# Performance work log

Measured on AMD Instinct MI355X. Metric: run time of the kernel, lower is better.

## Reference

```python
import jax, jax.numpy as jnp
import numpy as np

B, L, C, D, H = 32, 4096, 64, 512, 720
EPS = 1e-5

def _xavier(key, shape):
    fan_in, fan_out = shape
    lim = float(np.sqrt(6.0 / (fan_in + fan_out)))
    return jax.random.uniform(key, shape, minval=-lim, maxval=lim, dtype=jnp.float32)

def setup_inputs() -> dict:
    key = jax.random.key(0)
    ks = jax.random.split(key, 8)
    return {
        "x": jax.random.normal(ks[0], (B, L, C), dtype=jnp.float32),
        "alpha": jnp.full((C,), 0.5, dtype=jnp.float32),
        "rev_w": jnp.ones((C,), dtype=jnp.float32),
        "rev_b": jnp.zeros((C,), dtype=jnp.float32),
        "se_w": _xavier(ks[1], (C, D)), "se_b": jnp.zeros((D,), jnp.float32),
        "sp_w": _xavier(ks[2], (D, C)), "sp_b": jnp.zeros((C,), jnp.float32),
        "st_w": _xavier(ks[3], (L, H)), "st_b": jnp.zeros((H,), jnp.float32),
        "te_w": _xavier(ks[4], (C, D)), "te_b": jnp.zeros((D,), jnp.float32),
        "tp_w": _xavier(ks[5], (D, C)), "tp_b": jnp.zeros((C,), jnp.float32),
        "tt_w": _xavier(ks[6], (L, H)), "tt_b": jnp.zeros((H,), jnp.float32),
    }

def _path(z, ew, eb, pw, pb, tw, tb):
    # z: (B,L,C) -> embed C->D -> (identity backbone) -> proj D->C -> temporal L->H
    h = z @ ew + eb            # (B,L,D)
    h = h @ pw + pb            # (B,L,C)
    h = jnp.einsum('blc,lh->bhc', h, tw) + tb[None, :, None]  # (B,H,C)
    return h

def reference(x, alpha, rev_w, rev_b, se_w, se_b, sp_w, sp_b, st_w, st_b,
              te_w, te_b, tp_w, tp_b, tt_w, tt_b):
    # RevIN norm (stats detached, var unbiased=False)
    mean = jax.lax.stop_gradient(jnp.mean(x, axis=1, keepdims=True))          # (B,1,C)
    stdev = jax.lax.stop_gradient(jnp.sqrt(jnp.var(x, axis=1, keepdims=True) + EPS))
    xn = (x - mean) / stdev * rev_w + rev_b
    # EMA decomposition: trend[t] = a*trend[t-1] + (1-a)*x[t], trend[0]=x[0]
    a = jax.nn.sigmoid(alpha)  # (C,)
    def step(carry, xt):
        nxt = a * carry + (1.0 - a) * xt
        return nxt, nxt
    t0 = xn[:, 0]                                    # (B,C)
    _, tr = jax.lax.scan(step, t0, jnp.swapaxes(xn, 0, 1)[1:])  # (L-1,B,C)
    trend = jnp.swapaxes(jnp.concatenate([t0[None], tr], axis=0), 0, 1)  # (B,L,C)
    seasonal = xn - trend
    out = _path(seasonal, se_w, se_b, sp_w, sp_b, st_w, st_b) \
        + _path(trend,    te_w, te_b, tp_w, tp_b, tt_w, tt_b)   # (B,H,C)
    # RevIN denorm
    out = (out - rev_b) / (rev_w + EPS)
    out = out * stdev + mean
    return out
```

## Files before the change

### kernel.cpp

```cpp
#include <hip/hip_runtime.h>
#include <hip/hip_bf16.h>
#include <string.h>
#include <stdint.h>

typedef __hip_bfloat16 bf16_t;
typedef float f32x4 __attribute__((ext_vector_type(4)));
typedef short bf16x8 __attribute__((ext_vector_type(8)));

static constexpr int Bn = 32, Ln = 4096, Cn = 64, Hn = 720, HPn = 768;
static constexpr float EPSf = 1e-5f;

static constexpr size_t OSR_SLICE = (size_t)Bn * Hn * Cn;

__device__ __forceinline__ short f2bf(float f) {
  bf16_t h = __float2bfloat16(f);
  unsigned short u; memcpy(&u, &h, 2);
  return (short)u;
}

__device__ __forceinline__ float sigm(float v) { return 1.f / (1.f + expf(-v)); }

__global__ void __launch_bounds__(256) k_preA(
    const float* __restrict__ st_w, const float* __restrict__ tt_w,
    const float* __restrict__ x, const float* __restrict__ alpha,
    bf16_t* __restrict__ Wt, float* __restrict__ Spart,
    float* __restrict__ Psub, float* __restrict__ Pseg,
    float* __restrict__ Ssum, float* __restrict__ Ssq) {
  __shared__ __align__(16) char smem[20736];
  int bid = blockIdx.x, t = threadIdx.x;

  if (bid < 1536) {
    float (*tile)[65] = (float(*)[65])smem;
    float (*cs16)[64] = (float(*)[64])(smem + 16640);
    int p = bid / 768, rem = bid % 768;
    int lc = rem & 63, hc = rem >> 6;
    const float* W = p ? tt_w : st_w;
    int l0 = lc * 64, h0 = hc * 64;
    int g16 = t >> 4, c4l = (t & 15) * 4;
    int h = h0 + c4l;
    f32x4 ps = (f32x4){0.f, 0.f, 0.f, 0.f};
#pragma unroll
    for (int rr = 0; rr < 4; ++rr) {
      int r = rr * 16 + g16;
      const float* src = &W[(size_t)(l0 + r) * Hn + h];
      f32x4 v;
      if (h + 3 < Hn) {
        v = *reinterpret_cast<const f32x4*>(src);
      } else {
#pragma unroll
        for (int i = 0; i < 4; ++i) v[i] = (h + i < Hn) ? src[i] : 0.f;
      }
      tile[r][c4l + 0] = v[0]; tile[r][c4l + 1] = v[1];
      tile[r][c4l + 2] = v[2]; tile[r][c4l + 3] = v[3];
      ps += v;
    }
    *reinterpret_cast<f32x4*>(&cs16[g16][c4l]) = ps;
    __syncthreads();
    if (t < 64) {
      float s = 0.f;
#pragma unroll
      for (int g = 0; g < 16; ++g) s += cs16[g][t];
      Spart[((size_t)p * 64 + lc) * 768 + h0 + t] = s;
    }
    short* AF = (short*)Wt + (size_t)p * HPn * Ln;
#pragma unroll
    for (int u = 0; u < 2; ++u) {
      int uid = u * 256 + t;
      int ln = uid & 63, ktl = (uid >> 6) & 1, htl = uid >> 7;
      int fr = ln & 15, hi = ln >> 4;
      int ll = ktl * 32 + hi * 8;
      int hh = htl * 16 + fr;
      bf16x8 v;
#pragma unroll
      for (int e = 0; e < 8; ++e) v[e] = f2bf(tile[ll + e][hh]);
      size_t ht = (size_t)(h0 >> 4) + htl, ktg = (size_t)(l0 >> 5) + ktl;
      *reinterpret_cast<bf16x8*>(&AF[((ht * 128 + ktg) << 9) + ((size_t)ln << 3)]) = v;
    }
  } else {
    float (*lp)[64] = (float(*)[64])smem;
    float (*ls)[64] = (float(*)[64])(smem + 4096);
    float (*lq)[64] = (float(*)[64])(smem + 8192);
    int idx = bid - 1536;
    int b = idx >> 4, sg = idx & 15;
    int ty = t >> 6, tx = t & 63;
    int s = sg * 4 + ty;
    int c4 = (tx & 15) * 4, sub = tx >> 4;
    float a[4], k1[4];
#pragma unroll
    for (int i = 0; i < 4; ++i) { a[i] = sigm(alpha[c4 + i]); k1[i] = 1.f - a[i]; }
    const float* xb = x + ((size_t)b * Ln + s * 64 + sub * 16) * Cn + c4;
    float pr[4] = {0.f, 0.f, 0.f, 0.f}, sm[4] = {0.f, 0.f, 0.f, 0.f}, sq[4] = {0.f, 0.f, 0.f, 0.f};
#pragma unroll
    for (int j = 0; j < 16; ++j) {
      f32x4 v = *reinterpret_cast<const f32x4*>(xb + (size_t)j * Cn);
#pragma unroll
      for (int i = 0; i < 4; ++i) {
        sm[i] += v[i];
        sq[i] = fmaf(v[i], v[i], sq[i]);
        pr[i] = fmaf(a[i], pr[i], k1[i] * v[i]);
      }
    }
    *reinterpret_cast<f32x4*>(&Psub[(((size_t)b * 64 + s) * 4 + sub) * 64 + c4]) =
        (f32x4){pr[0], pr[1], pr[2], pr[3]};
#pragma unroll
    for (int i = 0; i < 4; ++i) {
      lp[ty * 4 + sub][c4 + i] = pr[i];
      ls[ty * 4 + sub][c4 + i] = sm[i];
      lq[ty * 4 + sub][c4 + i] = sq[i];
    }
    __syncthreads();
    int c = tx;
    float av = sigm(alpha[c]);
    float a16 = av * av; a16 *= a16; a16 *= a16; a16 *= a16;
    float P = ((lp[ty * 4 + 0][c] * a16 + lp[ty * 4 + 1][c]) * a16 + lp[ty * 4 + 2][c]) * a16 + lp[ty * 4 + 3][c];
    int oidx = (b * 64 + s) * 64 + c;
    Pseg[oidx] = P;
    Ssum[oidx] = ls[ty * 4 + 0][c] + ls[ty * 4 + 1][c] + ls[ty * 4 + 2][c] + ls[ty * 4 + 3][c];
    Ssq[oidx]  = lq[ty * 4 + 0][c] + lq[ty * 4 + 1][c] + lq[ty * 4 + 2][c] + lq[ty * 4 + 3][c];
  }
}

__global__ void __launch_bounds__(256) k_mid(
    const float* __restrict__ x, const float* __restrict__ alpha,
    const float* __restrict__ rev_w, const float* __restrict__ rev_b,
    const float* __restrict__ Pseg, const float* __restrict__ Ssum, const float* __restrict__ Ssq,
    const float* __restrict__ se_w, const float* __restrict__ sp_w,
    const float* __restrict__ se_b, const float* __restrict__ sp_b,
    const float* __restrict__ te_w, const float* __restrict__ tp_w,
    const float* __restrict__ te_b, const float* __restrict__ tp_b,
    const float* __restrict__ Spart,
    float* __restrict__ mean, float* __restrict__ rstd, float* __restrict__ stdv,
    float* __restrict__ CarryIn, float* __restrict__ M, float* __restrict__ cvec,
    float* __restrict__ S) {
  __shared__ __align__(16) char smem[35072];
  int bid = blockIdx.x, t = threadIdx.x;

  if (bid < 8) {
    int b = bid * 4 + (t >> 6), c = t & 63;
    float sm = 0.f, sq = 0.f;
#pragma unroll 8
    for (int s = 0; s < 64; ++s) {
      int idx = (b * 64 + s) * 64 + c;
      sm += Ssum[idx]; sq += Ssq[idx];
    }
    float mn = sm * (1.f / 4096.f);
    float var = sq * (1.f / 4096.f) - mn * mn;
    float sd = sqrtf(var + EPSf);
    float rs = 1.f / sd;
    mean[b * 64 + c] = mn; stdv[b * 64 + c] = sd; rstd[b * 64 + c] = rs;

    float w = rev_w[c], rb = rev_b[c];
    float g = rs * w, d = rb - mn * g;
    float a = sigm(alpha[c]);
    float a2 = a * a, a4 = a2 * a2, a8 = a4 * a4, a16 = a8 * a8, a32 = a16 * a16;
    float a64 = a32 * a32;
    float dk1s = d * (1.f - a64);
    float carry = fmaf(g, x[((size_t)b * Ln) * Cn + c], d);
    for (int so = 0; so < 8; ++so) {
      float pv[8];
#pragma unroll
      for (int i = 0; i < 8; ++i)
        pv[i] = Pseg[((size_t)(b * 64 + so * 8 + i)) * 64 + c];
#pragma unroll
      for (int i = 0; i < 8; ++i) {
        CarryIn[((size_t)(b * 64 + so * 8 + i)) * 64 + c] = carry;
        carry = fmaf(a64, carry, fmaf(g, pv[i], dk1s));
      }
    }
  } else if (bid < 10) {
    float (*ews)[68] = (float(*)[68])smem;
    float (*pws)[68] = (float(*)[68])(smem + 17408);
    float* ebs = (float*)(smem + 34816);
    int p = bid - 8;
    const float* ew = p ? te_w : se_w;
    const float* pw = p ? tp_w : sp_w;
    const float* eb = p ? te_b : se_b;
    const float* pb = p ? tp_b : sp_b;
    int r0 = (t >> 4) * 4, c0 = (t & 15) * 4;
    float acc[4][4];
#pragma unroll
    for (int i = 0; i < 4; ++i)
#pragma unroll
      for (int j = 0; j < 4; ++j) acc[i][j] = 0.f;
    float cv = 0.f;
    for (int dc = 0; dc < 8; ++dc) {
      int d0 = dc * 64;
#pragma unroll
      for (int q = 0; q < 4; ++q) {
        int fi = t * 4 + q;
        int r = fi >> 4, dd = (fi * 4) & 63;
        *reinterpret_cast<f32x4*>(&ews[r][dd]) = *reinterpret_cast<const f32x4*>(&ew[r * 512 + d0 + dd]);
        *reinterpret_cast<f32x4*>(&pws[r][dd]) = *reinterpret_cast<const f32x4*>(&pw[(d0 + r) * 64 + dd]);
      }
      if (t < 64) ebs[t] = eb[d0 + t];
      __syncthreads();
#pragma unroll 4
      for (int g = 0; g < 16; ++g) {
        int dd = g * 4;
        f32x4 av[4], bv[4];
#pragma unroll
        for (int i = 0; i < 4; ++i) av[i] = *reinterpret_cast<const f32x4*>(&ews[r0 + i][dd]);
#pragma unroll
        for (int d = 0; d < 4; ++d) bv[d] = *reinterpret_cast<const f32x4*>(&pws[dd + d][c0]);
#pragma unroll
        for (int d = 0; d < 4; ++d)
#pragma unroll
          for (int i = 0; i < 4; ++i)
#pragma unroll
            for (int j = 0; j < 4; ++j) acc[i][j] = fmaf(av[i][d], bv[d][j], acc[i][j]);
      }
      if (t < 64) {
#pragma unroll 8
        for (int dd = 0; dd < 64; ++dd) cv = fmaf(ebs[dd], pws[dd][t], cv);
      }
      __syncthreads();
    }
#pragma unroll
    for (int i = 0; i < 4; ++i)
#pragma unroll
      for (int j = 0; j < 4; ++j)
        M[p * 4096 + (r0 + i) * 64 + c0 + j] = acc[i][j];
    if (t < 64) cvec[p * 64 + t] = cv + pb[t];
  } else {
    int idx = (bid - 10) * 256 + t;
    int p = idx / 768, h = idx % 768;
    float s = 0.f;
#pragma unroll 8
    for (int lc = 0; lc < 64; ++lc)
      s += Spart[((size_t)p * 64 + lc) * 768 + h];
    S[p * 768 + h] = s;
  }
}

__global__ void __launch_bounds__(256) k_scanC(const float* __restrict__ x, const float* __restrict__ alpha,
                                               const float* __restrict__ rev_w, const float* __restrict__ rev_b,
                                               const float* __restrict__ mean, const float* __restrict__ rstd,
                                               const float* __restrict__ CarryIn, const float* __restrict__ Psub,
                                               bf16_t* __restrict__ Zt) {
  int b = blockIdx.x, ty = threadIdx.y, s = blockIdx.y * 4 + ty, t = threadIdx.x;
  int c4 = (t & 15) * 4, sub = t >> 4;
  float g[4], d[4], a[4], k1[4], a16[4], dk[4], tr[4];
#pragma unroll
  for (int i = 0; i < 4; ++i) {
    int c = c4 + i;
    float rs = rstd[b * 64 + c];
    g[i] = rs * rev_w[c]; d[i] = rev_b[c] - mean[b * 64 + c] * g[i];
    a[i] = sigm(alpha[c]); k1[i] = 1.f - a[i];
    float v = a[i] * a[i]; v *= v; v *= v; v *= v;
    a16[i] = v;
    dk[i] = d[i] * (1.f - v);
  }
  f32x4 cs = *reinterpret_cast<const f32x4*>(&CarryIn[((size_t)b * 64 + s) * 64 + c4]);
#pragma unroll
  for (int i = 0; i < 4; ++i) tr[i] = cs[i];
  for (int k = 0; k < sub; ++k) {
    f32x4 p = *reinterpret_cast<const f32x4*>(&Psub[(((size_t)b * 64 + s) * 4 + k) * 64 + c4]);
#pragma unroll
    for (int i = 0; i < 4; ++i) tr[i] = fmaf(a16[i], tr[i], fmaf(g[i], p[i], dk[i]));
  }
  const float* xb = x + ((size_t)b * Ln + s * 64 + sub * 16) * Cn + c4;
  bf16x8 vs[4][2], vt[4][2];
#pragma unroll
  for (int j = 0; j < 16; ++j) {
    f32x4 v = *reinterpret_cast<const f32x4*>(xb + (size_t)j * Cn);
#pragma unroll
    for (int i = 0; i < 4; ++i) {
      float xn = fmaf(g[i], v[i], d[i]);
      tr[i] = fmaf(a[i], tr[i], k1[i] * xn);
      vs[i][j >> 3][j & 7] = f2bf(xn - tr[i]);
      vt[i][j >> 3][j & 7] = f2bf(tr[i]);
    }
  }
  __shared__ short stage[4][8][520];
  short* BF0 = (short*)Zt;
  const size_t PATH = (size_t)Bn * Cn * Ln;
  int cq = (t & 15) >> 2;
  int u = cq * 2 + (sub >> 1);
  int hb = (sub & 1) * 2;
#pragma unroll
  for (int i = 0; i < 4; ++i) {
    int frv = (c4 & 15) + i;
    *reinterpret_cast<bf16x8*>(&stage[ty][u][(hb * 16 + frv) * 8]) = vs[i][0];
    *reinterpret_cast<bf16x8*>(&stage[ty][u][((hb + 1) * 16 + frv) * 8]) = vs[i][1];
  }
#pragma unroll
  for (int uu = 0; uu < 8; ++uu) {
    size_t nt = (size_t)b * 4 + (uu >> 1), ktg = (size_t)s * 2 + (uu & 1);
    *reinterpret_cast<bf16x8*>(BF0 + ((nt * 128 + ktg) << 9) + ((size_t)t << 3)) =
        *reinterpret_cast<const bf16x8*>(&stage[ty][uu][t * 8]);
  }
#pragma unroll
  for (int i = 0; i < 4; ++i) {
    int frv = (c4 & 15) + i;
    *reinterpret_cast<bf16x8*>(&stage[ty][u][(hb * 16 + frv) * 8]) = vt[i][0];
    *reinterpret_cast<bf16x8*>(&stage[ty][u][((hb + 1) * 16 + frv) * 8]) = vt[i][1];
  }
#pragma unroll
  for (int uu = 0; uu < 8; ++uu) {
    size_t nt = (size_t)b * 4 + (uu >> 1), ktg = (size_t)s * 2 + (uu & 1);
    *reinterpret_cast<bf16x8*>(BF0 + PATH + ((nt * 128 + ktg) << 9) + ((size_t)t << 3)) =
        *reinterpret_cast<const bf16x8*>(&stage[ty][uu][t * 8]);
  }
}

template <int KS>
__global__ void __launch_bounds__(256, 3) k_gemm(const bf16_t* __restrict__ Wt, const bf16_t* __restrict__ Zt,
                                                 float* __restrict__ Osr) {
  int per = gridDim.x >> 3;
  int swz = (blockIdx.x & 7) * per + (blockIdx.x >> 3);
  int z = swz / 96, rem = swz % 96;
  int by = rem >> 4, bx = rem & 15;
  int p = z / KS, kq = z % KS;
  const short* AF = (const short*)Wt + (size_t)p * HPn * Ln;
  const short* BF = (const short*)Zt + (size_t)p * (Bn * Cn) * Ln;
  int h0 = by * 128, n0 = bx * 128;
  int kbase = kq * (Ln / KS);
  const int NT = (Ln / KS) / 32;
  int tid = threadIdx.x, wid = tid >> 6, lane = tid & 63;
  int wr = wid >> 1, wc = wid & 1;
  int fr = lane & 15, hi = lane >> 4;
  const short* ab = AF + ((((size_t)(h0 >> 4) + wr * 4) * 128 + (kbase >> 5)) << 9) + ((size_t)lane << 3);
  const short* bb = BF + ((((size_t)(n0 >> 4) + wc * 4) * 128 + (kbase >> 5)) << 9) + ((size_t)lane << 3);

  f32x4 acc[4][4];
#pragma unroll
  for (int i = 0; i < 4; ++i)
#pragma unroll
    for (int j = 0; j < 4; ++j) acc[i][j] = (f32x4){0.f, 0.f, 0.f, 0.f};

  auto LOAD = [&](bf16x8 (&a)[4], bf16x8 (&b)[4], int kt) {
#pragma unroll
    for (int i = 0; i < 4; ++i)
      a[i] = *reinterpret_cast<const bf16x8*>(ab + (((size_t)i * 128 + kt) << 9));
#pragma unroll
    for (int j = 0; j < 4; ++j)
      b[j] = *reinterpret_cast<const bf16x8*>(bb + (((size_t)j * 128 + kt) << 9));
  };
  auto COMPUTE = [&](const bf16x8 (&a)[4], const bf16x8 (&b)[4]) {
    __builtin_amdgcn_s_setprio(1);
#pragma unroll
    for (int i = 0; i < 4; ++i)
#pragma unroll
      for (int j = 0; j < 4; ++j)
        acc[i][j] = __builtin_amdgcn_mfma_f32_16x16x32_bf16(a[i], b[j], acc[i][j], 0, 0, 0);
    __builtin_amdgcn_s_setprio(0);
  };

  bf16x8 aA[4], bA[4], aB[4], bB[4];
  LOAD(aA, bA, 0);
  for (int t = 0; t < NT; t += 2) {
    if (t + 1 < NT) LOAD(aB, bB, t + 1);
    __builtin_amdgcn_s_barrier();
    COMPUTE(aA, bA);
    if (t + 2 < NT) LOAD(aA, bA, t + 2);
    __builtin_amdgcn_s_barrier();
    if (t + 1 < NT) COMPUTE(aB, bB);
  }

#pragma unroll
  for (int i = 0; i < 4; ++i) {
#pragma unroll
    for (int j = 0; j < 4; ++j) {
#pragma unroll
      for (int r = 0; r < 4; ++r) {
        int m = wr * 64 + i * 16 + hi * 4 + r;
        int h = h0 + m;
        if (h < Hn) {
          int n = n0 + wc * 64 + j * 16 + fr;
          int bidx = n >> 6, c = n & 63;
          Osr[(((size_t)z * Bn + bidx) * Hn + h) * Cn + c] = acc[i][j][r];
        }
      }
    }
  }
}

template <int KS>
__global__ void __launch_bounds__(256) k_epi(const float* __restrict__ Osr, const float* __restrict__ M,
                                             const float* __restrict__ cvec, const float* __restrict__ S,
                                             const float* __restrict__ st_b, const float* __restrict__ tt_b,
                                             const float* __restrict__ rev_w, const float* __restrict__ rev_b,
                                             const float* __restrict__ mean, const float* __restrict__ stdv,
                                             float* __restrict__ out) {
  __shared__ float Msh[2][64][64];
  __shared__ float rowS[32][64];
  __shared__ float rowT[32][64];
  int t = threadIdx.x;
  for (int i = t; i < 2048; i += 256)
    reinterpret_cast<f32x4*>(Msh)[i] = reinterpret_cast<const f32x4*>(M)[i];
  int c = t & 63, grp = t >> 6;
  float w = rev_w[c], rb = rev_b[c];
  float cs = cvec[c], ct = cvec[64 + c];
  int base = blockIdx.x * 32;
#pragma unroll
  for (int k = 0; k < 8; ++k) {
    int rl = grp * 8 + k;
    int r = base + rl;
    int b = r / 720, h = r % 720;
    float vs = 0.f, vt = 0.f;
#pragma unroll
    for (int kq = 0; kq < KS; ++kq) {
      vs += Osr[(((size_t)kq * Bn + b) * Hn + h) * Cn + c];
      vt += Osr[(((size_t)(KS + kq) * Bn + b) * Hn + h) * Cn + c];
    }
    rowS[rl][c] = vs;
    rowT[rl][c] = vt;
  }
  __syncthreads();
  float acc[8];
  int hh[8], bb[8];
#pragma unroll
  for (int k = 0; k < 8; ++k) {
    int r = base + grp * 8 + k;
    bb[k] = r / 720; hh[k] = r % 720;
    acc[k] = cs * S[hh[k]] + ct * S[768 + hh[k]] + st_b[hh[k]] + tt_b[hh[k]];
  }
  int r0 = grp * 8;
  for (int cq = 0; cq < 16; ++cq) {
    f32x4 rs[8], rt[8];
#pragma unroll
    for (int k = 0; k < 8; ++k) rs[k] = *reinterpret_cast<const f32x4*>(&rowS[r0 + k][cq * 4]);
#pragma unroll
    for (int k = 0; k < 8; ++k) rt[k] = *reinterpret_cast<const f32x4*>(&rowT[r0 + k][cq * 4]);
#pragma unroll
    for (int i = 0; i < 4; ++i) {
      float m0 = Msh[0][cq * 4 + i][c], m1 = Msh[1][cq * 4 + i][c];
#pragma unroll
      for (int k = 0; k < 8; ++k)
        acc[k] = fmaf(rs[k][i], m0, fmaf(rt[k][i], m1, acc[k]));
    }
  }
  float winv = 1.f / (w + EPSf);
#pragma unroll
  for (int k = 0; k < 8; ++k) {
    float o = (acc[k] - rb) * winv * stdv[bb[k] * Cn + c] + mean[bb[k] * Cn + c];
    out[(size_t)(base + r0 + k) * 64 + c] = o;
  }
}

extern "C" void kernel_launch(void* const* d_in, const int* in_sizes, int n_in,
                              void* d_out, int out_size, void* d_ws, size_t ws_size,
                              hipStream_t stream) {
  const float* x     = (const float*)d_in[0];
  const float* alpha = (const float*)d_in[1];
  const float* rev_w = (const float*)d_in[2];
  const float* rev_b = (const float*)d_in[3];
  const float* se_w  = (const float*)d_in[4];
  const float* se_b  = (const float*)d_in[5];
  const float* sp_w  = (const float*)d_in[6];
  const float* sp_b  = (const float*)d_in[7];
  const float* st_w  = (const float*)d_in[8];
  const float* st_b  = (const float*)d_in[9];
  const float* te_w  = (const float*)d_in[10];
  const float* te_b  = (const float*)d_in[11];
  const float* tp_w  = (const float*)d_in[12];
  const float* tp_b  = (const float*)d_in[13];
  const float* tt_w  = (const float*)d_in[14];
  const float* tt_b  = (const float*)d_in[15];
  float* out = (float*)d_out;

  const size_t SZ_WT  = (size_t)2 * HPn * Ln * 2;
  const size_t SZ_ZT  = (size_t)2 * Bn * Cn * Ln * 2;
  const size_t SZ_SEG = (size_t)Bn * 64 * 64 * 4;
  const size_t SZ_M   = 2 * 64 * 64 * 4;
  const size_t SZ_CV  = 2 * 64 * 4;
  const size_t SZ_S   = 2 * 768 * 4;
  const size_t SZ_SP  = (size_t)2 * 64 * 768 * 4;
  const size_t TAIL   = SZ_M + SZ_CV + SZ_S + SZ_SP + 3 * (size_t)Bn * Cn * 4;

  const size_t NEED4 = SZ_WT + SZ_ZT + 8 * OSR_SLICE * 4 + TAIL;
  const int KS = (ws_size >= NEED4) ? 4 : 1;
  const size_t SZ_OSR = (size_t)(2 * KS) * OSR_SLICE * 4;

  char* ws = (char*)d_ws;
  bf16_t* Wt   = (bf16_t*)(ws);
  bf16_t* Zt   = (bf16_t*)(ws + SZ_WT);
  float*  Osr  = (float*)(ws + SZ_WT + SZ_ZT);
  float*  Psub  = Osr;
  float*  Pseg  = (float*)((char*)Psub + 4 * SZ_SEG);
  float*  Ssum  = (float*)((char*)Pseg + SZ_SEG);
  float*  Ssq   = (float*)((char*)Ssum + SZ_SEG);
  float*  Carry = (float*)((char*)Ssq + SZ_SEG);
  char* tail = ws + SZ_WT + SZ_ZT + SZ_OSR;
  float* Mbuf = (float*)tail;                 tail += SZ_M;
  float* cvec = (float*)tail;                 tail += SZ_CV;
  float* S    = (float*)tail;                 tail += SZ_S;
  float* Spart = (float*)tail;                tail += SZ_SP;
  float* mean = (float*)tail;                 tail += (size_t)Bn * Cn * 4;
  float* rstd = (float*)tail;                 tail += (size_t)Bn * Cn * 4;
  float* stdv = (float*)tail;

  k_preA<<<2048, 256, 0, stream>>>(st_w, tt_w, x, alpha, Wt, Spart, Psub, Pseg, Ssum, Ssq);
  k_mid<<<16, 256, 0, stream>>>(x, alpha, rev_w, rev_b, Pseg, Ssum, Ssq,
                                se_w, sp_w, se_b, sp_b, te_w, tp_w, te_b, tp_b, Spart,
                                mean, rstd, stdv, Carry, Mbuf, cvec, S);
  k_scanC<<<dim3(32, 16), dim3(64, 4), 0, stream>>>(x, alpha, rev_w, rev_b, mean, rstd, Carry, Psub, Zt);
  if (KS == 4) {
    k_gemm<4><<<768, 256, 0, stream>>>(Wt, Zt, Osr);
    k_epi<4><<<720, 256, 0, stream>>>(Osr, Mbuf, cvec, S, st_b, tt_b, rev_w, rev_b, mean, stdv, out);
  } else {
    k_gemm<1><<<192, 256, 0, stream>>>(Wt, Zt, Osr);
    k_epi<1><<<720, 256, 0, stream>>>(Osr, Mbuf, cvec, S, st_b, tt_b, rev_w, rev_b, mean, stdv, out);
  }
}
```

Measured before the change: 109.1 us.

## Store split-K partials in fp16 and deepen GEMM register pipeline to three stages

The GEMM now writes its split-K partial outputs as fp16 instead of fp32, and the epilogue reads them as fp16, which halves the traffic for the intermediate partial buffer. The GEMM main loop moves from two-stage to three-stage register prefetching without barriers, and the occupancy hint drops from 3 to 2 blocks per SM to make room for the extra registers. The workspace layout is adjusted so the scratch region used by the earlier kernels stays large enough. The cost is fp16 rounding and range limits on the partial sums, plus lower occupancy.

```diff
diff --git a/kernel.cpp b/kernel.cpp
--- a/kernel.cpp
+++ b/kernel.cpp
@@ -1,5 +1,6 @@
 #include <hip/hip_runtime.h>
 #include <hip/hip_bf16.h>
+#include <hip/hip_fp16.h>
 #include <string.h>
 #include <stdint.h>
 
@@ -304,8 +305,8 @@
 }
 
 template <int KS>
-__global__ void __launch_bounds__(256, 3) k_gemm(const bf16_t* __restrict__ Wt, const bf16_t* __restrict__ Zt,
-                                                 float* __restrict__ Osr) {
+__global__ void __launch_bounds__(256, 2) k_gemm(const bf16_t* __restrict__ Wt, const bf16_t* __restrict__ Zt,
+                                                 __half* __restrict__ Osr) {
   int per = gridDim.x >> 3;
   int swz = (blockIdx.x & 7) * per + (blockIdx.x >> 3);
   int z = swz / 96, rem = swz % 96;
@@ -346,15 +347,16 @@
     __builtin_amdgcn_s_setprio(0);
   };
 
-  bf16x8 aA[4], bA[4], aB[4], bB[4];
-  LOAD(aA, bA, 0);
-  for (int t = 0; t < NT; t += 2) {
-    if (t + 1 < NT) LOAD(aB, bB, t + 1);
-    __builtin_amdgcn_s_barrier();
-    COMPUTE(aA, bA);
-    if (t + 2 < NT) LOAD(aA, bA, t + 2);
-    __builtin_amdgcn_s_barrier();
-    if (t + 1 < NT) COMPUTE(aB, bB);
+  bf16x8 a0[4], b0[4], a1[4], b1[4], a2[4], b2[4];
+  LOAD(a0, b0, 0);
+  if (NT > 1) LOAD(a1, b1, 1);
+  for (int t = 0; t < NT; t += 3) {
+    if (t + 2 < NT) LOAD(a2, b2, t + 2);
+    COMPUTE(a0, b0);
+    if (t + 3 < NT) LOAD(a0, b0, t + 3);
+    if (t + 1 < NT) COMPUTE(a1, b1);
+    if (t + 4 < NT) LOAD(a1, b1, t + 4);
+    if (t + 2 < NT) COMPUTE(a2, b2);
   }
 
 #pragma unroll
@@ -368,7 +370,7 @@
         if (h < Hn) {
           int n = n0 + wc * 64 + j * 16 + fr;
           int bidx = n >> 6, c = n & 63;
-          Osr[(((size_t)z * Bn + bidx) * Hn + h) * Cn + c] = acc[i][j][r];
+          Osr[(((size_t)z * Bn + bidx) * Hn + h) * Cn + c] = __float2half(acc[i][j][r]);
         }
       }
     }
@@ -376,7 +378,7 @@
 }
 
 template <int KS>
-__global__ void __launch_bounds__(256) k_epi(const float* __restrict__ Osr, const float* __restrict__ M,
+__global__ void __launch_bounds__(256) k_epi(const __half* __restrict__ Osr, const float* __restrict__ M,
                                              const float* __restrict__ cvec, const float* __restrict__ S,
                                              const float* __restrict__ st_b, const float* __restrict__ tt_b,
                                              const float* __restrict__ rev_w, const float* __restrict__ rev_b,
@@ -400,8 +402,8 @@
     float vs = 0.f, vt = 0.f;
 #pragma unroll
     for (int kq = 0; kq < KS; ++kq) {
-      vs += Osr[(((size_t)kq * Bn + b) * Hn + h) * Cn + c];
-      vt += Osr[(((size_t)(KS + kq) * Bn + b) * Hn + h) * Cn + c];
+      vs += __half2float(Osr[(((size_t)kq * Bn + b) * Hn + h) * Cn + c]);
+      vt += __half2float(Osr[(((size_t)(KS + kq) * Bn + b) * Hn + h) * Cn + c]);
     }
     rowS[rl][c] = vs;
     rowT[rl][c] = vt;
@@ -468,15 +470,17 @@
   const size_t SZ_SP  = (size_t)2 * 64 * 768 * 4;
   const size_t TAIL   = SZ_M + SZ_CV + SZ_S + SZ_SP + 3 * (size_t)Bn * Cn * 4;
 
-  const size_t NEED4 = SZ_WT + SZ_ZT + 8 * OSR_SLICE * 4 + TAIL;
+  const size_t NEED4 = SZ_WT + SZ_ZT + 8 * OSR_SLICE * 2 + TAIL;
   const int KS = (ws_size >= NEED4) ? 4 : 1;
-  const size_t SZ_OSR = (size_t)(2 * KS) * OSR_SLICE * 4;
+  size_t SZ_OSR = (size_t)(2 * KS) * OSR_SLICE * 2;
+  const size_t SZ_SCRATCH = 4 * SZ_SEG + 4 * SZ_SEG;
+  if (SZ_OSR < SZ_SCRATCH) SZ_OSR = SZ_SCRATCH;
 
   char* ws = (char*)d_ws;
   bf16_t* Wt   = (bf16_t*)(ws);
   bf16_t* Zt   = (bf16_t*)(ws + SZ_WT);
-  float*  Osr  = (float*)(ws + SZ_WT + SZ_ZT);
-  float*  Psub  = Osr;
+  __half* Osr  = (__half*)(ws + SZ_WT + SZ_ZT);
+  float*  Psub  = (float*)Osr;
   float*  Pseg  = (float*)((char*)Psub + 4 * SZ_SEG);
   float*  Ssum  = (float*)((char*)Pseg + SZ_SEG);
   float*  Ssq   = (float*)((char*)Ssum + SZ_SEG);
```

Result: no change. 108.3 us (-0.7%).
